# Kernel optimization log

Measured on AMD Instinct MI355X. Metric: run time of the kernel, lower is better.

Reference implementation:

```python
import jax, jax.numpy as jnp
import numpy as np

B, S, D = 2, 2048, 2048
N_HEADS, N_KV_HEADS = 16, 4
HEAD_DIM = D // N_HEADS


def setup_inputs() -> dict:
    key = jax.random.key(0)
    ks = jax.random.split(key, 5)
    x = jax.random.normal(ks[0], (B, S, D), dtype=jnp.float32)
    W_q = jax.random.normal(ks[1], (D, D), dtype=jnp.float32) * 0.02
    W_k = jax.random.normal(ks[2], (D, N_KV_HEADS * HEAD_DIM), dtype=jnp.float32) * 0.02
    W_v = jax.random.normal(ks[3], (D, N_KV_HEADS * HEAD_DIM), dtype=jnp.float32) * 0.02
    W_o = jax.random.normal(ks[4], (D, D), dtype=jnp.float32) * 0.02
    return {"x": x, "W_q": W_q, "W_k": W_k, "W_v": W_v, "W_o": W_o}


def _apply_rope(xh, positions):
    # xh: [B, H, S, Dh]; rotate adjacent pairs as complex numbers
    Dh = xh.shape[-1]
    half = Dh // 2
    freqs = 1.0 / (10000.0 ** (jnp.arange(half, dtype=jnp.float32) / half))  # [half]
    angles = positions[:, None].astype(jnp.float32) * freqs[None, :]          # [S, half]
    cos, sin = jnp.cos(angles), jnp.sin(angles)
    xp = xh.reshape(*xh.shape[:-1], half, 2)
    x0, x1 = xp[..., 0], xp[..., 1]
    r0 = x0 * cos - x1 * sin
    r1 = x0 * sin + x1 * cos
    return jnp.stack([r0, r1], axis=-1).reshape(xh.shape)


def reference(x, W_q, W_k, W_v, W_o):
    b, s, d = x.shape
    positions = jnp.arange(s)
    rep = N_HEADS // N_KV_HEADS
    Q = (x @ W_q).reshape(b, s, N_HEADS, HEAD_DIM).transpose(0, 2, 1, 3)        # [B,H,S,Dh]
    K = (x @ W_k).reshape(b, s, N_KV_HEADS, HEAD_DIM).transpose(0, 2, 1, 3)     # [B,Hkv,S,Dh]
    V = (x @ W_v).reshape(b, s, N_KV_HEADS, HEAD_DIM).transpose(0, 2, 1, 3)
    Qr = _apply_rope(Q, positions)
    # torch .repeat(1, rep, 1, 1) tiles kv-head blocks: head h -> kv head h % n_kv_heads
    K_rep = jnp.tile(K, (1, rep, 1, 1))
    V_rep = jnp.tile(V, (1, rep, 1, 1))
    Kr = _apply_rope(K_rep, positions)
    scores = jnp.einsum('bhqd,bhkd->bhqk', Qr, Kr) / (HEAD_DIM ** 0.5)
    weights = jax.nn.softmax(scores, axis=-1)
    out = jnp.einsum('bhqk,bhkd->bhqd', weights, V_rep)
    out = out.transpose(0, 2, 1, 3).reshape(b, s, d)
    return out @ W_o
```

## Files before the change

### kernel.cpp

```cpp
#include <hip/hip_runtime.h>


typedef __attribute__((ext_vector_type(8))) short  short8;
typedef __attribute__((ext_vector_type(8))) __bf16 bf16x8;
typedef __attribute__((ext_vector_type(4))) float  f32x4;

#define B_   2
#define S_   2048
#define D_   2048
#define H_   16
#define HKV_ 4
#define DH_  128
#define M_   4096
#define NQKV 3072

static __device__ __forceinline__ ushort f2bf(float f) {
  __bf16 h = (__bf16)f;
  return __builtin_bit_cast(unsigned short, h);
}
static __device__ __forceinline__ float bf2f(ushort u) {
  union { unsigned u; float f; } v; v.u = ((unsigned)u) << 16;
  return v.f;
}
static __device__ __forceinline__ f32x4 mfma16(short8 a, short8 b, f32x4 c) {
  return __builtin_amdgcn_mfma_f32_16x16x32_bf16(
      __builtin_bit_cast(bf16x8, a), __builtin_bit_cast(bf16x8, b), c, 0, 0, 0);
}
static __device__ __forceinline__ void gload16(const ushort* g, ushort* l) {
  __builtin_amdgcn_global_load_lds(
      (const __attribute__((address_space(1))) unsigned int*)g,
      (__attribute__((address_space(3))) unsigned int*)l, 16, 0, 0);
}
template <int N>
static __device__ __forceinline__ void vmwait() {
  asm volatile("s_waitcnt vmcnt(%0)" :: "n"(N) : "memory");
}

__global__ void conv_f32_bf16(const float* __restrict__ in,
                              ushort* __restrict__ out, int n4) {
  int i = blockIdx.x * blockDim.x + threadIdx.x;
  if (i >= n4) return;
  float4 v = ((const float4*)in)[i];
  ushort4 o;
  o.x = f2bf(v.x); o.y = f2bf(v.y); o.z = f2bf(v.z); o.w = f2bf(v.w);
  ((ushort4*)out)[i] = o;
}

__global__ void transpose_conv(const float* __restrict__ in,
                               ushort* __restrict__ out, int R, int C) {
  __shared__ float tile[32][33];
  int c0 = blockIdx.x * 32, r0 = blockIdx.y * 32;
  int tx = threadIdx.x, ty = threadIdx.y;
#pragma unroll
  for (int i = 0; i < 32; i += 8)
    tile[ty + i][tx] = in[(size_t)(r0 + ty + i) * C + c0 + tx];
  __syncthreads();
#pragma unroll
  for (int i = 0; i < 32; i += 8)
    out[(size_t)(c0 + ty + i) * R + r0 + tx] = f2bf(tile[tx][ty + i]);
}

__global__ void transpose_v(const ushort* __restrict__ in,
                            ushort* __restrict__ out, int src_stride) {
  __shared__ ushort tile[32][33];
  int bkv = blockIdx.z;
  const ushort* src = in + (size_t)(bkv >> 2) * S_ * src_stride + (bkv & 3) * DH_;
  ushort* dst = out + (size_t)bkv * DH_ * S_;
  int d0 = blockIdx.x * 32, s0 = blockIdx.y * 32;
  int tx = threadIdx.x, ty = threadIdx.y;
#pragma unroll
  for (int i = 0; i < 32; i += 8)
    tile[ty + i][tx] = src[(size_t)(s0 + ty + i) * src_stride + d0 + tx];
  __syncthreads();
#pragma unroll
  for (int i = 0; i < 32; i += 8)
    dst[(size_t)(d0 + ty + i) * S_ + s0 + tx] = tile[tx][ty + i];
}

__global__ void rope_table_k(float2* __restrict__ tab) {
  int i = blockIdx.x * blockDim.x + threadIdx.x;
  int pos = i >> 6, f = i & 63;
  float freq = powf(10000.0f, -(float)f / 64.0f);
  float a = (float)pos * freq;
  tab[i] = make_float2(cosf(a), sinf(a));
}

__global__ void rope_apply_k(ushort* __restrict__ t,
                             const float2* __restrict__ tab,
                             int total, int ppr_shift, int row_stride,
                             float oscale) {
  int idx = blockIdx.x * blockDim.x + threadIdx.x;
  if (idx >= total) return;
  int row = idx >> ppr_shift;
  int p   = idx & ((1 << ppr_shift) - 1);
  int head = p >> 6, fi = p & 63;
  int pos = row & (S_ - 1);
  float2 cs = tab[(pos << 6) + fi];
  size_t off = (size_t)row * row_stride + head * DH_ + 2 * fi;
  ushort2 v = *(ushort2*)&t[off];
  float x0 = bf2f(v.x), x1 = bf2f(v.y);
  ushort2 o;
  o.x = f2bf((x0 * cs.x - x1 * cs.y) * oscale);
  o.y = f2bf((x0 * cs.y + x1 * cs.x) * oscale);
  *(ushort2*)&t[off] = o;
}

template <int BN, int NF, typename OutT>
__global__ __launch_bounds__(512, 1) void gemm8p(const ushort* __restrict__ A,
                                                 const ushort* __restrict__ Bt,
                                                 OutT* __restrict__ C,
                                                 int M, int N, int K) {
  __shared__ ushort As[2][256 * 64];
  __shared__ ushort Bs[2][BN * 64];
  const int tid = threadIdx.x;
  const int lane = tid & 63, w = tid >> 6;
  const int l16 = lane & 15, l4 = lane >> 4;
  const int wm = (w >> 2) * 128, wn = (w & 3) * (BN / 4);
  const int bm = blockIdx.x * 256, bn = blockIdx.y * BN;
  const int swz = l16 & 7;

  const ushort* gA = A  + (size_t)bm * K;
  const ushort* gB = Bt + (size_t)bn * K;
  const int srow = tid >> 3;
  const int scb  = tid & 7;
  const int sswz = srow & 7;

  auto stageA = [&](int t, int s, int g) {
    int row = g * 64 + srow;
    gload16(gA + (size_t)row * K + t * 64 + ((scb ^ sswz) * 8),
            &As[s][(g * 64 + w * 8) * 64]);
  };
  auto stageB = [&](int t, int s, int g) {
    int row = g * 64 + srow;
    gload16(gB + (size_t)row * K + t * 64 + ((scb ^ sswz) * 8),
            &Bs[s][(g * 64 + w * 8) * 64]);
  };
  auto stageB2 = [&](int t, int s) {
    if constexpr (NF == 3) stageB(t, s, 2);
  };

  constexpr int VM_A = (NF == 3) ? 9 : 8;
  constexpr int VM_B = (NF == 3) ? 7 : 6;

  f32x4 acc[8][NF] = {};
  short8 bfr[NF][2];
  const int NT  = K / 64;
  const int NIT = K / 128;

  stageB(0, 0, 0); stageB(0, 0, 1); stageB2(0, 0);
  stageA(0, 0, 0); stageA(0, 0, 2);
  stageA(0, 0, 1); stageA(0, 0, 3);
  stageB(1, 1, 0); stageB(1, 1, 1); stageB2(1, 1);
  stageA(1, 1, 0); stageA(1, 1, 2);
  vmwait<VM_B>();
  __builtin_amdgcn_s_barrier();
  __builtin_amdgcn_sched_barrier(0);

#define GPHASE(S, J, ISSUES, VMW)                                             \
  {                                                                           \
    short8 afr[2][2];                                                         \
    _Pragma("unroll")                                                         \
    for (int mf = 0; mf < 2; ++mf) {                                          \
      _Pragma("unroll")                                                       \
      for (int kk = 0; kk < 2; ++kk) {                                        \
        int row = wm + (J) * 32 + mf * 16 + l16;                              \
        afr[mf][kk] =                                                         \
            *(const short8*)&As[S][row * 64 + (((kk * 4 + l4) ^ swz) * 8)];   \
      }                                                                       \
    }                                                                         \
    if ((J) == 0) {                                                           \
      _Pragma("unroll")                                                       \
      for (int nf = 0; nf < NF; ++nf) {                                       \
        _Pragma("unroll")                                                     \
        for (int kk = 0; kk < 2; ++kk) {                                      \
          int row = wn + nf * 16 + l16;                                       \
          bfr[nf][kk] =                                                       \
              *(const short8*)&Bs[S][row * 64 + (((kk * 4 + l4) ^ swz) * 8)]; \
        }                                                                     \
      }                                                                       \
    }                                                                         \
    ISSUES;                                                                   \
    __builtin_amdgcn_s_barrier();                                             \
    asm volatile("s_waitcnt lgkmcnt(0)" ::: "memory");                        \
    __builtin_amdgcn_sched_barrier(0);                                        \
    __builtin_amdgcn_s_setprio(1);                                            \
    _Pragma("unroll")                                                         \
    for (int kk = 0; kk < 2; ++kk) {                                          \
      _Pragma("unroll")                                                       \
      for (int mf = 0; mf < 2; ++mf) {                                        \
        _Pragma("unroll")                                                     \
        for (int nf = 0; nf < NF; ++nf)                                       \
          acc[(J) * 2 + mf][nf] =                                             \
              mfma16(afr[mf][kk], bfr[nf][kk], acc[(J) * 2 + mf][nf]);        \
      }                                                                       \
    }                                                                         \
    __builtin_amdgcn_s_setprio(0);                                            \
    VMW;                                                                      \
    __builtin_amdgcn_s_barrier();                                             \
    __builtin_amdgcn_sched_barrier(0);                                        \
  }

  for (int i = 0; i < NIT; ++i) {
    const int tb  = 2 * i + 1;
    const int ta2 = (2 * i + 2 < NT) ? 2 * i + 2 : NT - 1;
    const int tb2 = (2 * i + 3 < NT) ? 2 * i + 3 : NT - 1;
    GPHASE(0, 0, (stageA(tb, 1, 1), stageA(tb, 1, 3)), (void)0)
    GPHASE(0, 1, (stageB(ta2, 0, 0), stageB(ta2, 0, 1)), vmwait<VM_A>())
    GPHASE(0, 2, (stageB2(ta2, 0), stageA(ta2, 0, 0)), (void)0)
    GPHASE(0, 3, (stageA(ta2, 0, 2)), vmwait<VM_B>())
    GPHASE(1, 0, (stageA(ta2, 0, 1), stageA(ta2, 0, 3)), (void)0)
    GPHASE(1, 1, (stageB(tb2, 1, 0), stageB(tb2, 1, 1)), vmwait<VM_A>())
    GPHASE(1, 2, (stageB2(tb2, 1), stageA(tb2, 1, 0)), (void)0)
    GPHASE(1, 3, (stageA(tb2, 1, 2)), vmwait<VM_B>())
  }
#undef GPHASE

  asm volatile("s_waitcnt vmcnt(0)" ::: "memory");

#pragma unroll
  for (int mi = 0; mi < 8; ++mi) {
#pragma unroll
    for (int nf = 0; nf < NF; ++nf) {
#pragma unroll
      for (int r = 0; r < 4; ++r) {
        size_t row = bm + wm + (mi >> 1) * 32 + (mi & 1) * 16 + l4 * 4 + r;
        size_t col = bn + wn + nf * 16 + l16;
        if constexpr (sizeof(OutT) == 2)
          C[row * N + col] = f2bf(acc[mi][nf][r]);
        else
          C[row * N + col] = acc[mi][nf][r];
      }
    }
  }
}

__global__ __launch_bounds__(256, 2) void flash_attn(const ushort* __restrict__ Qp,
                                                     const ushort* __restrict__ Kp,
                                                     const ushort* __restrict__ Vt,
                                                     ushort* __restrict__ Oa) {
  __shared__ ushort Ks[2][64 * 128];
  __shared__ ushort Vs[2][128 * 64];
  const int tid = threadIdx.x;
  const int lane = tid & 63, wave = tid >> 6;
  const int l16 = lane & 15, l4 = lane >> 4;
  const int bh = blockIdx.y;
  const int b = bh >> 4, h = bh & 15, kv = h & 3;
  const int q0 = blockIdx.x * 128 + wave * 32;

  short8 qf[2][4];
#pragma unroll
  for (int qg = 0; qg < 2; ++qg) {
    const ushort* qrow =
        Qp + ((size_t)(b * S_ + q0 + qg * 16 + l16)) * NQKV + h * DH_ + l4 * 8;
#pragma unroll
    for (int kk = 0; kk < 4; ++kk) qf[qg][kk] = *(const short8*)(qrow + kk * 32);
  }

  const ushort* kbase = Kp + (size_t)(b * S_) * NQKV + kv * DH_;
  const ushort* vbase = Vt + (size_t)(b * HKV_ + kv) * DH_ * S_;

  float mreg[2] = {-1e30f, -1e30f}, lsum[2] = {0.f, 0.f};
  f32x4 o[2][8] = {};

  const int kswz = (l16 & 3) | (((l16 >> 2) & 1) << 2);
  const int vswz = l16 & 7;

  const int krT = wave * 16 + (lane >> 4);
  const int kcT = lane & 15;
  const int vrT = wave * 32 + (lane >> 3);
  const int vcT = lane & 7;

  auto stage = [&](int t, int buf) {
#pragma unroll
    for (int i = 0; i < 4; ++i) {
      int r = krT + i * 4;
      int swzk = (r & 3) | (((r >> 3) & 1) << 2);
      gload16(kbase + (size_t)(t * 64 + r) * NQKV + ((kcT ^ swzk) * 8),
              &Ks[buf][(wave * 16 + i * 4) * 128]);
      int d = vrT + i * 8;
      gload16(vbase + (size_t)d * S_ + t * 64 + ((vcT ^ (d & 7)) * 8),
              &Vs[buf][(wave * 32 + i * 8) * 64]);
    }
  };

  const int NT = S_ / 64;
  stage(0, 0);
  __syncthreads();

  for (int t = 0; t < NT; ++t) {
    const int cur = t & 1;
    if (t + 1 < NT) stage(t + 1, cur ^ 1);

    f32x4 s[2][4] = {};
    __builtin_amdgcn_s_setprio(1);
#pragma unroll
    for (int c = 0; c < 4; ++c) {
      const int krow = 32 * (c >> 1) + 8 * (l16 >> 2) + 4 * (c & 1) + (l16 & 3);
#pragma unroll
      for (int kk = 0; kk < 4; ++kk) {
        short8 kf = *(const short8*)&Ks[cur][krow * 128 + (((kk * 4 + l4) ^ kswz) * 8)];
        s[0][c] = mfma16(kf, qf[0][kk], s[0][c]);
        s[1][c] = mfma16(kf, qf[1][kk], s[1][c]);
      }
    }
    __builtin_amdgcn_s_setprio(0);

    float tmax[2];
#pragma unroll
    for (int qg = 0; qg < 2; ++qg) {
      float a = fmaxf(fmaxf(s[qg][0][0], s[qg][0][1]), fmaxf(s[qg][0][2], s[qg][0][3]));
#pragma unroll
      for (int c = 1; c < 4; ++c) {
        a = fmaxf(a, fmaxf(fmaxf(s[qg][c][0], s[qg][c][1]),
                           fmaxf(s[qg][c][2], s[qg][c][3])));
      }
      a = fmaxf(a, __shfl_xor(a, 16));
      tmax[qg] = fmaxf(a, __shfl_xor(a, 32));
    }

    bool ok = (tmax[0] - mreg[0] <= 8.0f) && (tmax[1] - mreg[1] <= 8.0f);
    if (!__all(ok)) {
#pragma unroll
      for (int qg = 0; qg < 2; ++qg) {
        float mn = fmaxf(mreg[qg], tmax[qg]);
        float alpha = __builtin_amdgcn_exp2f(mreg[qg] - mn);
        mreg[qg] = mn;
        lsum[qg] *= alpha;
        float af[4];
#pragma unroll
        for (int r = 0; r < 4; ++r)
          af[r] = __shfl(alpha, (lane & 48) + l4 * 4 + r);
#pragma unroll
        for (int g = 0; g < 8; ++g)
#pragma unroll
          for (int r = 0; r < 4; ++r) o[qg][g][r] *= af[r];
      }
    }

    short8 pa[2][2];
    float rs[2] = {0.f, 0.f};
#pragma unroll
    for (int qg = 0; qg < 2; ++qg) {
#pragma unroll
      for (int ks = 0; ks < 2; ++ks) {
        short8 pk;
#pragma unroll
        for (int j = 0; j < 8; ++j) {
          float p = __builtin_amdgcn_exp2f(s[qg][2 * ks + (j >> 2)][j & 3] - mreg[qg]);
          rs[qg] += p;
          pk[j] = (short)f2bf(p);
        }
        pa[qg][ks] = pk;
      }
      float r2 = rs[qg] + __shfl_xor(rs[qg], 16);
      lsum[qg] += r2 + __shfl_xor(r2, 32);
    }

    __builtin_amdgcn_s_setprio(1);
#pragma unroll
    for (int ks = 0; ks < 2; ++ks) {
#pragma unroll
      for (int g = 0; g < 8; ++g) {
        const int d = g * 16 + l16;
        short8 vf = *(const short8*)&Vs[cur][d * 64 + (((ks * 4 + l4) ^ vswz) * 8)];
        o[0][g] = mfma16(pa[0][ks], vf, o[0][g]);
        o[1][g] = mfma16(pa[1][ks], vf, o[1][g]);
      }
    }
    __builtin_amdgcn_s_setprio(0);

    __syncthreads();
  }

#pragma unroll
  for (int qg = 0; qg < 2; ++qg) {
    float inv = 1.0f / lsum[qg];
    float invq[4];
#pragma unroll
    for (int r = 0; r < 4; ++r)
      invq[r] = __shfl(inv, (lane & 48) + l4 * 4 + r);
    ushort* op = Oa + (size_t)(b * S_ + q0 + qg * 16) * D_ + h * DH_;
#pragma unroll
    for (int g = 0; g < 8; ++g)
#pragma unroll
      for (int r = 0; r < 4; ++r)
        op[(size_t)(l4 * 4 + r) * D_ + g * 16 + l16] = f2bf(o[qg][g][r] * invq[r]);
  }
}

extern "C" void kernel_launch(void* const* d_in, const int* in_sizes, int n_in,
                              void* d_out, int out_size, void* d_ws, size_t ws_size,
                              hipStream_t stream) {
  (void)in_sizes; (void)n_in; (void)out_size; (void)ws_size;
  const float* x  = (const float*)d_in[0];
  const float* Wq = (const float*)d_in[1];
  const float* Wk = (const float*)d_in[2];
  const float* Wv = (const float*)d_in[3];
  const float* Wo = (const float*)d_in[4];
  float* out = (float*)d_out;

  size_t off = 0;
  auto carve = [&](size_t bytes) -> void* {
    void* p = (char*)d_ws + off;
    off += (bytes + 255) & ~(size_t)255;
    return p;
  };
  ushort* xb    = (ushort*)carve((size_t)M_ * D_ * 2);
  ushort* Wqkvt = (ushort*)carve((size_t)NQKV * D_ * 2);
  ushort* Wot   = (ushort*)carve((size_t)D_ * D_ * 2);
  ushort* QKV   = (ushort*)carve((size_t)M_ * NQKV * 2);
  ushort* Vt    = (ushort*)carve((size_t)M_ * 512 * 2);
  ushort* attn  = (ushort*)carve((size_t)M_ * D_ * 2);
  float2* tab   = (float2*)carve((size_t)S_ * 64 * sizeof(float2));

  conv_f32_bf16<<<(M_ * D_ / 4 + 255) / 256, 256, 0, stream>>>(x, xb, M_ * D_ / 4);
  transpose_conv<<<dim3(64, 64), dim3(32, 8), 0, stream>>>(Wq, Wqkvt, 2048, 2048);
  transpose_conv<<<dim3(16, 64), dim3(32, 8), 0, stream>>>(Wk, Wqkvt + (size_t)2048 * 2048, 2048, 512);
  transpose_conv<<<dim3(16, 64), dim3(32, 8), 0, stream>>>(Wv, Wqkvt + (size_t)2560 * 2048, 2048, 512);
  transpose_conv<<<dim3(64, 64), dim3(32, 8), 0, stream>>>(Wo, Wot, 2048, 2048);
  rope_table_k<<<(S_ * 64) / 256, 256, 0, stream>>>(tab);

  gemm8p<192, 3, ushort><<<dim3(16, 16), 512, 0, stream>>>(xb, Wqkvt, QKV, M_, NQKV, 2048);

  const float qscale = 0.08838834764831845f * 1.4426950408889634f;
  rope_apply_k<<<(M_ * 1024) / 256, 256, 0, stream>>>(QKV, tab, M_ * 1024, 10, NQKV, qscale);
  rope_apply_k<<<(M_ * 256) / 256, 256, 0, stream>>>(QKV + 2048, tab, M_ * 256, 8, NQKV, 1.0f);
  transpose_v<<<dim3(4, 64, 8), dim3(32, 8), 0, stream>>>(QKV + 2560, Vt, NQKV);

  flash_attn<<<dim3(S_ / 128, B_ * H_), 256, 0, stream>>>(QKV, QKV + 2048, Vt, attn);

  gemm8p<128, 2, float><<<dim3(16, 16), 512, 0, stream>>>(attn, Wot, out, M_, 2048, 2048);
}
```

Baseline: 219.5 us.

## Fuse RoPE into QKV GEMM epilogue and interleave softmax with PV MFMAs

Removes the two standalone RoPE kernels and applies the rotation and Q scaling in the QKV GEMM store epilogue. The adjacent-pair partner comes from a lane shuffle and cos/sin from the precomputed table. This saves a read-modify-write pass over Q and K and two launches, but adds per-element table loads and branches to the epilogue. In flash attention, exp/pack for each k-slice now runs just before that slice's PV MFMAs, and the row-sum reductions move after them, which shortens register live ranges and may let softmax overlap with matrix work.

```diff
diff --git a/kernel.cpp b/kernel.cpp
--- a/kernel.cpp
+++ b/kernel.cpp
@@ -85,31 +85,13 @@
   tab[i] = make_float2(cosf(a), sinf(a));
 }
 
-__global__ void rope_apply_k(ushort* __restrict__ t,
-                             const float2* __restrict__ tab,
-                             int total, int ppr_shift, int row_stride,
-                             float oscale) {
-  int idx = blockIdx.x * blockDim.x + threadIdx.x;
-  if (idx >= total) return;
-  int row = idx >> ppr_shift;
-  int p   = idx & ((1 << ppr_shift) - 1);
-  int head = p >> 6, fi = p & 63;
-  int pos = row & (S_ - 1);
-  float2 cs = tab[(pos << 6) + fi];
-  size_t off = (size_t)row * row_stride + head * DH_ + 2 * fi;
-  ushort2 v = *(ushort2*)&t[off];
-  float x0 = bf2f(v.x), x1 = bf2f(v.y);
-  ushort2 o;
-  o.x = f2bf((x0 * cs.x - x1 * cs.y) * oscale);
-  o.y = f2bf((x0 * cs.y + x1 * cs.x) * oscale);
-  *(ushort2*)&t[off] = o;
-}
-
-template <int BN, int NF, typename OutT>
+template <int BN, int NF, bool ROPE, typename OutT>
 __global__ __launch_bounds__(512, 1) void gemm8p(const ushort* __restrict__ A,
                                                  const ushort* __restrict__ Bt,
                                                  OutT* __restrict__ C,
-                                                 int M, int N, int K) {
+                                                 int M, int N, int K,
+                                                 const float2* __restrict__ tab,
+                                                 float qsc) {
   __shared__ ushort As[2][256 * 64];
   __shared__ ushort Bs[2][BN * 64];
   const int tid = threadIdx.x;
@@ -225,10 +207,20 @@
       for (int r = 0; r < 4; ++r) {
         size_t row = bm + wm + (mi >> 1) * 32 + (mi & 1) * 16 + l4 * 4 + r;
         size_t col = bn + wn + nf * 16 + l16;
+        float v = acc[mi][nf][r];
+        if constexpr (ROPE) {
+          float part = __shfl_xor(v, 1);
+          if ((int)col < 2560) {
+            float2 cs = tab[(((int)row & (S_ - 1)) << 6) + (((int)col & 127) >> 1)];
+            float o_ = v * cs.x + part * ((l16 & 1) ? cs.y : -cs.y);
+            if ((int)col < 2048) o_ *= qsc;
+            v = o_;
+          }
+        }
         if constexpr (sizeof(OutT) == 2)
-          C[row * N + col] = f2bf(acc[mi][nf][r]);
+          C[row * N + col] = f2bf(v);
         else
-          C[row * N + col] = acc[mi][nf][r];
+          C[row * N + col] = v;
       }
     }
   }
@@ -337,12 +329,12 @@
       }
     }
 
-    short8 pa[2][2];
     float rs[2] = {0.f, 0.f};
-#pragma unroll
-    for (int qg = 0; qg < 2; ++qg) {
-#pragma unroll
-      for (int ks = 0; ks < 2; ++ks) {
+    short8 pa[2];
+#pragma unroll
+    for (int ks = 0; ks < 2; ++ks) {
+#pragma unroll
+      for (int qg = 0; qg < 2; ++qg) {
         short8 pk;
 #pragma unroll
         for (int j = 0; j < 8; ++j) {
@@ -350,24 +342,23 @@
           rs[qg] += p;
           pk[j] = (short)f2bf(p);
         }
-        pa[qg][ks] = pk;
-      }
-      float r2 = rs[qg] + __shfl_xor(rs[qg], 16);
-      lsum[qg] += r2 + __shfl_xor(r2, 32);
-    }
-
-    __builtin_amdgcn_s_setprio(1);
-#pragma unroll
-    for (int ks = 0; ks < 2; ++ks) {
+        pa[qg] = pk;
+      }
+      __builtin_amdgcn_s_setprio(1);
 #pragma unroll
       for (int g = 0; g < 8; ++g) {
         const int d = g * 16 + l16;
         short8 vf = *(const short8*)&Vs[cur][d * 64 + (((ks * 4 + l4) ^ vswz) * 8)];
-        o[0][g] = mfma16(pa[0][ks], vf, o[0][g]);
-        o[1][g] = mfma16(pa[1][ks], vf, o[1][g]);
-      }
-    }
-    __builtin_amdgcn_s_setprio(0);
+        o[0][g] = mfma16(pa[0], vf, o[0][g]);
+        o[1][g] = mfma16(pa[1], vf, o[1][g]);
+      }
+      __builtin_amdgcn_s_setprio(0);
+    }
+#pragma unroll
+    for (int qg = 0; qg < 2; ++qg) {
+      float r2 = rs[qg] + __shfl_xor(rs[qg], 16);
+      lsum[qg] += r2 + __shfl_xor(r2, 32);
+    }
 
     __syncthreads();
   }
@@ -420,14 +411,14 @@
   transpose_conv<<<dim3(64, 64), dim3(32, 8), 0, stream>>>(Wo, Wot, 2048, 2048);
   rope_table_k<<<(S_ * 64) / 256, 256, 0, stream>>>(tab);
 
-  gemm8p<192, 3, ushort><<<dim3(16, 16), 512, 0, stream>>>(xb, Wqkvt, QKV, M_, NQKV, 2048);
-
   const float qscale = 0.08838834764831845f * 1.4426950408889634f;
-  rope_apply_k<<<(M_ * 1024) / 256, 256, 0, stream>>>(QKV, tab, M_ * 1024, 10, NQKV, qscale);
-  rope_apply_k<<<(M_ * 256) / 256, 256, 0, stream>>>(QKV + 2048, tab, M_ * 256, 8, NQKV, 1.0f);
+  gemm8p<192, 3, true, ushort><<<dim3(16, 16), 512, 0, stream>>>(
+      xb, Wqkvt, QKV, M_, NQKV, 2048, tab, qscale);
+
   transpose_v<<<dim3(4, 64, 8), dim3(32, 8), 0, stream>>>(QKV + 2560, Vt, NQKV);
 
   flash_attn<<<dim3(S_ / 128, B_ * H_), 256, 0, stream>>>(QKV, QKV + 2048, Vt, attn);
 
-  gemm8p<128, 2, float><<<dim3(16, 16), 512, 0, stream>>>(attn, Wot, out, M_, 2048, 2048);
-}
+  gemm8p<128, 2, false, float><<<dim3(16, 16), 512, 0, stream>>>(
+      attn, Wot, out, M_, 2048, 2048, nullptr, 1.0f);
+}
```

Result: no change. 223.6 us (+1.9%).
